# Kernel tuning notes

Measured on AMD Instinct MI355X. Metric: run time of the kernel, lower is better.

The kernel has to match this reference:

```python
import jax, jax.numpy as jnp
import numpy as np

B, T, C = 4, 2048, 1024
H = 16
D = C // H  # head_dim = 64


def setup_inputs() -> dict:
    key = jax.random.key(0)
    k1, k2, k3, k4, k5 = jax.random.split(key, 5)
    s = 0.02
    return {
        "x": jax.random.normal(k1, (B, T, C), dtype=jnp.float32),
        "W_qkv": jax.random.normal(k2, (C, 3 * C), dtype=jnp.float32) * s,
        "b_qkv": jax.random.normal(k3, (3 * C,), dtype=jnp.float32) * s,
        "W_o": jax.random.normal(k4, (C, C), dtype=jnp.float32) * s,
        "b_o": jax.random.normal(k5, (C,), dtype=jnp.float32) * s,
    }


def reference(x, W_qkv, b_qkv, W_o, b_o):
    b, t, c = x.shape
    scaling = D ** (-0.5)
    qkv = x @ W_qkv + b_qkv                      # [B,T,3C]
    q, k, v = jnp.split(qkv, 3, axis=-1)         # each [B,T,C]
    q = q.reshape(b, t, H, D).transpose(0, 2, 1, 3)  # [B,H,T,D]
    k = k.reshape(b, t, H, D).transpose(0, 2, 1, 3)
    v = v.reshape(b, t, H, D).transpose(0, 2, 1, 3)
    scores = jnp.einsum("bhqd,bhkd->bhqk", q, k) * scaling  # [B,H,T,T]
    mask = jnp.tril(jnp.ones((t, t), dtype=bool))            # causal
    scores = jnp.where(mask[None, None, :, :], scores, -jnp.inf)
    probs = jax.nn.softmax(scores, axis=-1)
    out = jnp.einsum("bhqk,bhkd->bhqd", probs, v)            # [B,H,T,D]
    out = out.transpose(0, 2, 1, 3).reshape(b, t, c)         # [B,T,C]
    return out @ W_o + b_o
```

## Files before the change

### kernel.cpp

```cpp
#include <hip/hip_runtime.h>
#include <hip/hip_bf16.h>

typedef unsigned short ushort_t;
typedef __attribute__((ext_vector_type(8))) short short8;
typedef __attribute__((ext_vector_type(4))) float floatx4;

#define B_ 4
#define T_ 2048
#define C_ 1024
#define H_ 16
#define D_ 64
#define BT_ (B_ * T_)
#define N3C (3 * C_)

#define KSC 0.18033688011112042f

__device__ __forceinline__ ushort_t f2bf(float f) {
    unsigned u = __float_as_uint(f);
    u += 0x7FFF + ((u >> 16) & 1);
    return (ushort_t)(u >> 16);
}
__device__ __forceinline__ unsigned pack2bf(float a, float b) {
    __hip_bfloat162 h = __float22bfloat162_rn(make_float2(a, b));
    return *(unsigned*)&h;
}

__device__ __forceinline__ void gload16(const ushort_t* g, ushort_t* l) {
    __builtin_amdgcn_global_load_lds((const __attribute__((address_space(1))) void*)g,
                                     (__attribute__((address_space(3))) void*)l, 16, 0, 0);
}

__global__ void convert_x_k(const float* __restrict__ xin, ushort_t* __restrict__ xb) {
    size_t i = ((size_t)blockIdx.x * 256 + threadIdx.x) * 8;
    const float* xf = xin + i;
    float4 a = *(const float4*)xf;
    float4 b = *(const float4*)(xf + 4);
    short8 o;
    o[0] = (short)f2bf(a.x); o[1] = (short)f2bf(a.y);
    o[2] = (short)f2bf(a.z); o[3] = (short)f2bf(a.w);
    o[4] = (short)f2bf(b.x); o[5] = (short)f2bf(b.y);
    o[6] = (short)f2bf(b.z); o[7] = (short)f2bf(b.w);
    *(short8*)&xb[i] = o;
}

__global__ void transpose_k(const float* __restrict__ in, ushort_t* __restrict__ out,
                            int R, int Nc) {
    __shared__ ushort_t t[32][33];
    int bc = blockIdx.x * 32;
    int br = blockIdx.y * 32;
    int lx = threadIdx.x & 31, ly = threadIdx.x >> 5;
#pragma unroll
    for (int i = 0; i < 4; ++i) {
        int r = ly + i * 8;
        t[r][lx] = f2bf(in[(size_t)(br + r) * Nc + bc + lx]);
    }
    __syncthreads();
#pragma unroll
    for (int i = 0; i < 4; ++i) {
        int r = ly + i * 8;
        out[(size_t)(bc + r) * R + br + lx] = t[lx][r];
    }
}

__global__ void vtrans_k(const ushort_t* __restrict__ in, ushort_t* __restrict__ out) {
    __shared__ ushort_t t[32][33];
    int bh = blockIdx.z;
    const ushort_t* I = in + (size_t)bh * T_ * D_;
    ushort_t* O = out + (size_t)bh * D_ * T_;
    int bt = blockIdx.x * 32, bd = blockIdx.y * 32;
    int lx = threadIdx.x & 31, ly = threadIdx.x >> 5;
#pragma unroll
    for (int i = 0; i < 4; ++i) {
        int r = ly + i * 8;
        t[r][lx] = I[(size_t)(bt + r) * D_ + bd + lx];
    }
    __syncthreads();
#pragma unroll
    for (int i = 0; i < 4; ++i) {
        int r = ly + i * 8;
        O[(size_t)(bd + r) * T_ + bt + lx] = t[lx][r];
    }
}

template <int MODE>
__launch_bounds__(256)
__global__ void gemm_bt(const ushort_t* __restrict__ A, const ushort_t* __restrict__ Bt,
                        const float* __restrict__ bias, float* __restrict__ Cout,
                        ushort_t* __restrict__ Qo, ushort_t* __restrict__ Ko,
                        ushort_t* __restrict__ Vo, int M, int N, int K) {
    __shared__ __align__(16) ushort_t Alds[128 * 32];
    __shared__ __align__(16) ushort_t Blds[128 * 32];
    int tid = threadIdx.x;
    int wave = tid >> 6, lane = tid & 63;
    int bm = blockIdx.x * 128, bn = blockIdx.y * 128;
    int wr = (wave >> 1) * 64, wc = (wave & 1) * 64;
    int lm = lane & 15, lk = (lane >> 4) * 8, lq = lane >> 4;

    floatx4 acc[4][4] = {};

    int srow = tid >> 2;
    int scol = (tid & 3) * 8;
    const ushort_t* Ab = A + (size_t)(bm + srow) * K + scol;
    const ushort_t* Bb = Bt + (size_t)(bn + srow) * K + scol;
    ushort_t* Al0 = &Alds[wave * 512];
    ushort_t* Al1 = &Alds[2048 + wave * 512];
    ushort_t* Bl0 = &Blds[wave * 512];
    ushort_t* Bl1 = &Blds[2048 + wave * 512];
    size_t rowskip = (size_t)64 * K;

    for (int k0 = 0; k0 < K; k0 += 32) {
        __syncthreads();
        gload16(Ab + k0, Al0);
        gload16(Ab + k0 + rowskip, Al1);
        gload16(Bb + k0, Bl0);
        gload16(Bb + k0 + rowskip, Bl1);
        __syncthreads();
        short8 af[4], bf[4];
#pragma unroll
        for (int i = 0; i < 4; ++i)
            af[i] = *(const short8*)&Alds[(wr + i * 16 + lm) * 32 + lk];
#pragma unroll
        for (int i = 0; i < 4; ++i)
            bf[i] = *(const short8*)&Blds[(wc + i * 16 + lm) * 32 + lk];
#pragma unroll
        for (int mi = 0; mi < 4; ++mi)
#pragma unroll
            for (int ni = 0; ni < 4; ++ni)
                acc[mi][ni] = __builtin_amdgcn_mfma_f32_16x16x32_bf16(
                    af[mi], bf[ni], acc[mi][ni], 0, 0, 0);
    }

#pragma unroll
    for (int mi = 0; mi < 4; ++mi) {
#pragma unroll
        for (int ni = 0; ni < 4; ++ni) {
            int col = bn + wc + ni * 16 + lm;
            float bv = bias[col];
#pragma unroll
            for (int r = 0; r < 4; ++r) {
                int row = bm + wr + mi * 16 + lq * 4 + r;
                float v = acc[mi][ni][r] + bv;
                if (MODE == 0) {
                    Cout[(size_t)row * N + col] = v;
                } else {
                    int b = row >> 11, t = row & (T_ - 1);
                    int which = col >> 10, c = col & (C_ - 1);
                    int h = c >> 6, d = c & 63;
                    int bh = b * H_ + h;
                    size_t idx = ((size_t)bh * T_ + t) * D_ + d;
                    if (which == 0)
                        Qo[idx] = f2bf(v * KSC);
                    else if (which == 1)
                        Ko[idx] = f2bf(v);
                    else
                        Vo[idx] = f2bf(v);
                }
            }
        }
    }
}

__launch_bounds__(256)
__global__ void attn_k(const ushort_t* __restrict__ Q, const ushort_t* __restrict__ K,
                       const ushort_t* __restrict__ Vt, ushort_t* __restrict__ O) {
    __shared__ __align__(16) ushort_t Klds[64 * 72];
    __shared__ __align__(16) ushort_t Vlds[64 * 72];
    __shared__ __align__(16) ushort_t Plds[4][16 * 72];

    int tid = threadIdx.x, wave = tid >> 6, lane = tid & 63;
    int id = blockIdx.x;
    int xcd = id & 7, bx = (id >> 3) & 15, grp = id >> 7;
    int bh = xcd + 8 * grp;
    int b = bh >> 4, h = bh & 15;
    int lm = lane & 15, lq = lane >> 4;

    const ushort_t* Qp = Q + (size_t)bh * T_ * D_;
    const ushort_t* Kp = K + (size_t)bh * T_ * D_;
    const ushort_t* Vp = Vt + (size_t)bh * D_ * T_;
    ushort_t* Pw = &Plds[wave][0];
    ushort_t* Ob = O + ((size_t)b * T_) * C_ + h * D_;

    int srow = tid >> 2, scol = (tid & 3) * 16;
    const ushort_t* Kg = Kp + (size_t)srow * D_ + scol;
    const ushort_t* Vg = Vp + (size_t)srow * T_ + scol;
    ushort_t* Kl = &Klds[srow * 72 + scol];
    ushort_t* Vl = &Vlds[srow * 72 + scol];

    int prow = lm * 72 + lq * 4;
    int pread = lm * 72 + lq * 8;

    short8 onesf = {};
    if (lm == 0) {
#pragma unroll
        for (int j = 0; j < 8; ++j) onesf[j] = (short)0x3F80;
    }

#pragma unroll
    for (int pass = 0; pass < 2; ++pass) {
        int band = pass ? (31 - bx) : bx;
        int m0 = band * 64 + wave * 16;

        short8 qf0 = *(const short8*)&Qp[(size_t)(m0 + lm) * D_ + lq * 8];
        short8 qf1 = *(const short8*)&Qp[(size_t)(m0 + lm) * D_ + 32 + lq * 8];

        floatx4 oacc[5] = {};

        int ntw = band + 1;
        short8 kr0 = *(const short8*)Kg;
        short8 kr1 = *(const short8*)(Kg + 8);
        short8 vr0 = *(const short8*)Vg;
        short8 vr1 = *(const short8*)(Vg + 8);

        for (int it = 0; it < ntw; ++it) {
            __syncthreads();
            *(short8*)Kl = kr0;
            *(short8*)(Kl + 8) = kr1;
            *(short8*)Vl = vr0;
            *(short8*)(Vl + 8) = vr1;
            __syncthreads();

            if (it + 1 < ntw) {
                const ushort_t* kn = Kg + (size_t)(it + 1) * 64 * D_;
                const ushort_t* vn = Vg + (it + 1) * 64;
                kr0 = *(const short8*)kn;
                kr1 = *(const short8*)(kn + 8);
                vr0 = *(const short8*)vn;
                vr1 = *(const short8*)(vn + 8);
            }

            short8 kf[4][2], vf[4][2];
#pragma unroll
            for (int nt = 0; nt < 4; ++nt) {
                kf[nt][0] = *(const short8*)&Klds[(nt * 16 + lm) * 72 + lq * 8];
                kf[nt][1] = *(const short8*)&Klds[(nt * 16 + lm) * 72 + 32 + lq * 8];
            }

            floatx4 st[4] = {};
#pragma unroll
            for (int nt = 0; nt < 4; ++nt) {
                st[nt] = __builtin_amdgcn_mfma_f32_16x16x32_bf16(kf[nt][0], qf0, st[nt], 0, 0, 0);
                st[nt] = __builtin_amdgcn_mfma_f32_16x16x32_bf16(kf[nt][1], qf1, st[nt], 0, 0, 0);
            }

#pragma unroll
            for (int dt = 0; dt < 4; ++dt) {
                vf[dt][0] = *(const short8*)&Vlds[(dt * 16 + lm) * 72 + lq * 8];
                vf[dt][1] = *(const short8*)&Vlds[(dt * 16 + lm) * 72 + 32 + lq * 8];
            }

            int kv0 = it * 64;
            if (it == ntw - 1) {
                int mg = m0 + lm;
#pragma unroll
                for (int nt = 0; nt < 4; ++nt)
#pragma unroll
                    for (int r = 0; r < 4; ++r) {
                        int kvg = kv0 + nt * 16 + lq * 4 + r;
                        if (kvg > mg) st[nt][r] = -__builtin_inff();
                    }
            }

#pragma unroll
            for (int nt = 0; nt < 4; ++nt) {
                uint2 pk;
                pk.x = pack2bf(exp2f(st[nt][0]), exp2f(st[nt][1]));
                pk.y = pack2bf(exp2f(st[nt][2]), exp2f(st[nt][3]));
                *(uint2*)&Pw[prow + nt * 16] = pk;
            }

            asm volatile("s_waitcnt lgkmcnt(0)" ::: "memory");

            short8 pb0 = *(const short8*)&Pw[pread];
            short8 pb1 = *(const short8*)&Pw[pread + 32];
#pragma unroll
            for (int dt = 0; dt < 4; ++dt) {
                oacc[dt] = __builtin_amdgcn_mfma_f32_16x16x32_bf16(vf[dt][0], pb0, oacc[dt], 0, 0, 0);
                oacc[dt] = __builtin_amdgcn_mfma_f32_16x16x32_bf16(vf[dt][1], pb1, oacc[dt], 0, 0, 0);
            }
            oacc[4] = __builtin_amdgcn_mfma_f32_16x16x32_bf16(onesf, pb0, oacc[4], 0, 0, 0);
            oacc[4] = __builtin_amdgcn_mfma_f32_16x16x32_bf16(onesf, pb1, oacc[4], 0, 0, 0);
        }

        float li = __shfl(oacc[4][0], lm, 64);
        float inv = 1.0f / li;
        int tg = m0 + lm;
#pragma unroll
        for (int dt = 0; dt < 4; ++dt) {
            uint2 pk;
            pk.x = pack2bf(oacc[dt][0] * inv, oacc[dt][1] * inv);
            pk.y = pack2bf(oacc[dt][2] * inv, oacc[dt][3] * inv);
            *(uint2*)&Ob[(size_t)tg * C_ + dt * 16 + lq * 4] = pk;
        }
    }
}

extern "C" void kernel_launch(void* const* d_in, const int* in_sizes, int n_in,
                              void* d_out, int out_size, void* d_ws, size_t ws_size,
                              hipStream_t stream) {
    const float* x    = (const float*)d_in[0];
    const float* Wqkv = (const float*)d_in[1];
    const float* bqkv = (const float*)d_in[2];
    const float* Wo   = (const float*)d_in[3];
    const float* bo   = (const float*)d_in[4];

    ushort_t* ws = (ushort_t*)d_ws;
    ushort_t* WqkvT = ws;
    ushort_t* WoT   = WqkvT + (size_t)N3C * C_;
    ushort_t* Xb    = WoT + (size_t)C_ * C_;
    ushort_t* Qs    = Xb + (size_t)BT_ * C_;
    ushort_t* Ks    = Qs + (size_t)BT_ * C_;
    ushort_t* Vs    = Ks + (size_t)BT_ * C_;
    ushort_t* Attn  = Vs + (size_t)BT_ * C_;

    convert_x_k<<<BT_ * C_ / (256 * 8), 256, 0, stream>>>(x, Xb);
    transpose_k<<<dim3(N3C / 32, C_ / 32), 256, 0, stream>>>(Wqkv, WqkvT, C_, N3C);
    transpose_k<<<dim3(C_ / 32, C_ / 32), 256, 0, stream>>>(Wo, WoT, C_, C_);
    gemm_bt<1><<<dim3(BT_ / 128, N3C / 128), 256, 0, stream>>>(
        Xb, WqkvT, bqkv, nullptr, Qs, Ks, Attn, BT_, N3C, C_);
    vtrans_k<<<dim3(T_ / 32, D_ / 32, B_ * H_), 256, 0, stream>>>(Attn, Vs);
    attn_k<<<1024, 256, 0, stream>>>(Qs, Ks, Vs, Attn);
    gemm_bt<0><<<dim3(BT_ / 128, C_ / 128), 256, 0, stream>>>(
        Attn, WoT, bo, (float*)d_out, nullptr, nullptr, nullptr, BT_, C_, C_);
}
```

Before: 288.9 us.

## Replace LDS P round-trip with permlane swaps and launch one band per block

The attention kernel now rearranges the bf16 probability tile between MFMA layouts with permlane32/permlane16 swap instructions instead of writing it to shared memory and reading it back. This removes the P LDS buffer and a waitcnt stall. The grid also becomes one causal band per block (2048 blocks), ordered longest band first, instead of pairing short and long bands in one block. This trades the built-in load balance of pairing for more blocks and lower LDS use.

```diff
diff --git a/kernel.cpp b/kernel.cpp
--- a/kernel.cpp
+++ b/kernel.cpp
@@ -4,6 +4,8 @@
 typedef unsigned short ushort_t;
 typedef __attribute__((ext_vector_type(8))) short short8;
 typedef __attribute__((ext_vector_type(4))) float floatx4;
+typedef __attribute__((ext_vector_type(2))) unsigned uint2v;
+typedef __attribute__((ext_vector_type(4))) unsigned uint4v;
 
 #define B_ 4
 #define T_ 2048
@@ -165,19 +167,18 @@
                        const ushort_t* __restrict__ Vt, ushort_t* __restrict__ O) {
     __shared__ __align__(16) ushort_t Klds[64 * 72];
     __shared__ __align__(16) ushort_t Vlds[64 * 72];
-    __shared__ __align__(16) ushort_t Plds[4][16 * 72];
 
     int tid = threadIdx.x, wave = tid >> 6, lane = tid & 63;
     int id = blockIdx.x;
-    int xcd = id & 7, bx = (id >> 3) & 15, grp = id >> 7;
-    int bh = xcd + 8 * grp;
+    int xcd = id & 7, j = id >> 3;
+    int band = 31 - (j & 31);
+    int bh = xcd + 8 * (j >> 5);
     int b = bh >> 4, h = bh & 15;
     int lm = lane & 15, lq = lane >> 4;
 
     const ushort_t* Qp = Q + (size_t)bh * T_ * D_;
     const ushort_t* Kp = K + (size_t)bh * T_ * D_;
     const ushort_t* Vp = Vt + (size_t)bh * D_ * T_;
-    ushort_t* Pw = &Plds[wave][0];
     ushort_t* Ob = O + ((size_t)b * T_) * C_ + h * D_;
 
     int srow = tid >> 2, scol = (tid & 3) * 16;
@@ -186,111 +187,113 @@
     ushort_t* Kl = &Klds[srow * 72 + scol];
     ushort_t* Vl = &Vlds[srow * 72 + scol];
 
-    int prow = lm * 72 + lq * 4;
-    int pread = lm * 72 + lq * 8;
-
     short8 onesf = {};
     if (lm == 0) {
 #pragma unroll
-        for (int j = 0; j < 8; ++j) onesf[j] = (short)0x3F80;
-    }
-
-#pragma unroll
-    for (int pass = 0; pass < 2; ++pass) {
-        int band = pass ? (31 - bx) : bx;
-        int m0 = band * 64 + wave * 16;
-
-        short8 qf0 = *(const short8*)&Qp[(size_t)(m0 + lm) * D_ + lq * 8];
-        short8 qf1 = *(const short8*)&Qp[(size_t)(m0 + lm) * D_ + 32 + lq * 8];
-
-        floatx4 oacc[5] = {};
-
-        int ntw = band + 1;
-        short8 kr0 = *(const short8*)Kg;
-        short8 kr1 = *(const short8*)(Kg + 8);
-        short8 vr0 = *(const short8*)Vg;
-        short8 vr1 = *(const short8*)(Vg + 8);
-
-        for (int it = 0; it < ntw; ++it) {
-            __syncthreads();
-            *(short8*)Kl = kr0;
-            *(short8*)(Kl + 8) = kr1;
-            *(short8*)Vl = vr0;
-            *(short8*)(Vl + 8) = vr1;
-            __syncthreads();
-
-            if (it + 1 < ntw) {
-                const ushort_t* kn = Kg + (size_t)(it + 1) * 64 * D_;
-                const ushort_t* vn = Vg + (it + 1) * 64;
-                kr0 = *(const short8*)kn;
-                kr1 = *(const short8*)(kn + 8);
-                vr0 = *(const short8*)vn;
-                vr1 = *(const short8*)(vn + 8);
-            }
-
-            short8 kf[4][2], vf[4][2];
-#pragma unroll
-            for (int nt = 0; nt < 4; ++nt) {
-                kf[nt][0] = *(const short8*)&Klds[(nt * 16 + lm) * 72 + lq * 8];
-                kf[nt][1] = *(const short8*)&Klds[(nt * 16 + lm) * 72 + 32 + lq * 8];
-            }
-
-            floatx4 st[4] = {};
-#pragma unroll
-            for (int nt = 0; nt < 4; ++nt) {
-                st[nt] = __builtin_amdgcn_mfma_f32_16x16x32_bf16(kf[nt][0], qf0, st[nt], 0, 0, 0);
-                st[nt] = __builtin_amdgcn_mfma_f32_16x16x32_bf16(kf[nt][1], qf1, st[nt], 0, 0, 0);
-            }
-
-#pragma unroll
-            for (int dt = 0; dt < 4; ++dt) {
-                vf[dt][0] = *(const short8*)&Vlds[(dt * 16 + lm) * 72 + lq * 8];
-                vf[dt][1] = *(const short8*)&Vlds[(dt * 16 + lm) * 72 + 32 + lq * 8];
-            }
-
-            int kv0 = it * 64;
-            if (it == ntw - 1) {
-                int mg = m0 + lm;
-#pragma unroll
-                for (int nt = 0; nt < 4; ++nt)
-#pragma unroll
-                    for (int r = 0; r < 4; ++r) {
-                        int kvg = kv0 + nt * 16 + lq * 4 + r;
-                        if (kvg > mg) st[nt][r] = -__builtin_inff();
-                    }
-            }
-
-#pragma unroll
-            for (int nt = 0; nt < 4; ++nt) {
-                uint2 pk;
-                pk.x = pack2bf(exp2f(st[nt][0]), exp2f(st[nt][1]));
-                pk.y = pack2bf(exp2f(st[nt][2]), exp2f(st[nt][3]));
-                *(uint2*)&Pw[prow + nt * 16] = pk;
-            }
-
-            asm volatile("s_waitcnt lgkmcnt(0)" ::: "memory");
-
-            short8 pb0 = *(const short8*)&Pw[pread];
-            short8 pb1 = *(const short8*)&Pw[pread + 32];
-#pragma unroll
-            for (int dt = 0; dt < 4; ++dt) {
-                oacc[dt] = __builtin_amdgcn_mfma_f32_16x16x32_bf16(vf[dt][0], pb0, oacc[dt], 0, 0, 0);
-                oacc[dt] = __builtin_amdgcn_mfma_f32_16x16x32_bf16(vf[dt][1], pb1, oacc[dt], 0, 0, 0);
-            }
-            oacc[4] = __builtin_amdgcn_mfma_f32_16x16x32_bf16(onesf, pb0, oacc[4], 0, 0, 0);
-            oacc[4] = __builtin_amdgcn_mfma_f32_16x16x32_bf16(onesf, pb1, oacc[4], 0, 0, 0);
-        }
-
-        float li = __shfl(oacc[4][0], lm, 64);
-        float inv = 1.0f / li;
-        int tg = m0 + lm;
+        for (int jj = 0; jj < 8; ++jj) onesf[jj] = (short)0x3F80;
+    }
+
+    int m0 = band * 64 + wave * 16;
+
+    short8 qf0 = *(const short8*)&Qp[(size_t)(m0 + lm) * D_ + lq * 8];
+    short8 qf1 = *(const short8*)&Qp[(size_t)(m0 + lm) * D_ + 32 + lq * 8];
+
+    floatx4 oacc[5] = {};
+
+    int ntw = band + 1;
+    short8 kr0 = *(const short8*)Kg;
+    short8 kr1 = *(const short8*)(Kg + 8);
+    short8 vr0 = *(const short8*)Vg;
+    short8 vr1 = *(const short8*)(Vg + 8);
+
+    for (int it = 0; it < ntw; ++it) {
+        __syncthreads();
+        *(short8*)Kl = kr0;
+        *(short8*)(Kl + 8) = kr1;
+        *(short8*)Vl = vr0;
+        *(short8*)(Vl + 8) = vr1;
+        __syncthreads();
+
+        if (it + 1 < ntw) {
+            const ushort_t* kn = Kg + (size_t)(it + 1) * 64 * D_;
+            const ushort_t* vn = Vg + (it + 1) * 64;
+            kr0 = *(const short8*)kn;
+            kr1 = *(const short8*)(kn + 8);
+            vr0 = *(const short8*)vn;
+            vr1 = *(const short8*)(vn + 8);
+        }
+
+        short8 kf[4][2], vf[4][2];
+#pragma unroll
+        for (int nt = 0; nt < 4; ++nt) {
+            kf[nt][0] = *(const short8*)&Klds[(nt * 16 + lm) * 72 + lq * 8];
+            kf[nt][1] = *(const short8*)&Klds[(nt * 16 + lm) * 72 + 32 + lq * 8];
+        }
+
+        floatx4 st[4] = {};
+#pragma unroll
+        for (int nt = 0; nt < 4; ++nt) {
+            st[nt] = __builtin_amdgcn_mfma_f32_16x16x32_bf16(kf[nt][0], qf0, st[nt], 0, 0, 0);
+            st[nt] = __builtin_amdgcn_mfma_f32_16x16x32_bf16(kf[nt][1], qf1, st[nt], 0, 0, 0);
+        }
+
 #pragma unroll
         for (int dt = 0; dt < 4; ++dt) {
-            uint2 pk;
-            pk.x = pack2bf(oacc[dt][0] * inv, oacc[dt][1] * inv);
-            pk.y = pack2bf(oacc[dt][2] * inv, oacc[dt][3] * inv);
-            *(uint2*)&Ob[(size_t)tg * C_ + dt * 16 + lq * 4] = pk;
-        }
+            vf[dt][0] = *(const short8*)&Vlds[(dt * 16 + lm) * 72 + lq * 8];
+            vf[dt][1] = *(const short8*)&Vlds[(dt * 16 + lm) * 72 + 32 + lq * 8];
+        }
+
+        int kv0 = it * 64;
+        if (it == ntw - 1) {
+            int mg = m0 + lm;
+#pragma unroll
+            for (int nt = 0; nt < 4; ++nt)
+#pragma unroll
+                for (int r = 0; r < 4; ++r) {
+                    int kvg = kv0 + nt * 16 + lq * 4 + r;
+                    if (kvg > mg) st[nt][r] = -__builtin_inff();
+                }
+        }
+
+        unsigned e0 = pack2bf(exp2f(st[0][0]), exp2f(st[0][1]));
+        unsigned e1 = pack2bf(exp2f(st[0][2]), exp2f(st[0][3]));
+        unsigned e2 = pack2bf(exp2f(st[1][0]), exp2f(st[1][1]));
+        unsigned e3 = pack2bf(exp2f(st[1][2]), exp2f(st[1][3]));
+        unsigned e4 = pack2bf(exp2f(st[2][0]), exp2f(st[2][1]));
+        unsigned e5 = pack2bf(exp2f(st[2][2]), exp2f(st[2][3]));
+        unsigned e6 = pack2bf(exp2f(st[3][0]), exp2f(st[3][1]));
+        unsigned e7 = pack2bf(exp2f(st[3][2]), exp2f(st[3][3]));
+
+        uint2v ra = __builtin_amdgcn_permlane32_swap(e0, e2, false, false);
+        uint2v wa = __builtin_amdgcn_permlane16_swap(ra[0], ra[1], false, false);
+        uint2v rb = __builtin_amdgcn_permlane32_swap(e1, e3, false, false);
+        uint2v wb = __builtin_amdgcn_permlane16_swap(rb[0], rb[1], false, false);
+        uint2v rc = __builtin_amdgcn_permlane32_swap(e4, e6, false, false);
+        uint2v wc = __builtin_amdgcn_permlane16_swap(rc[0], rc[1], false, false);
+        uint2v rd = __builtin_amdgcn_permlane32_swap(e5, e7, false, false);
+        uint2v wd = __builtin_amdgcn_permlane16_swap(rd[0], rd[1], false, false);
+
+        short8 pb0 = __builtin_bit_cast(short8, (uint4v){wa[0], wb[0], wa[1], wb[1]});
+        short8 pb1 = __builtin_bit_cast(short8, (uint4v){wc[0], wd[0], wc[1], wd[1]});
+
+#pragma unroll
+        for (int dt = 0; dt < 4; ++dt) {
+            oacc[dt] = __builtin_amdgcn_mfma_f32_16x16x32_bf16(vf[dt][0], pb0, oacc[dt], 0, 0, 0);
+            oacc[dt] = __builtin_amdgcn_mfma_f32_16x16x32_bf16(vf[dt][1], pb1, oacc[dt], 0, 0, 0);
+        }
+        oacc[4] = __builtin_amdgcn_mfma_f32_16x16x32_bf16(onesf, pb0, oacc[4], 0, 0, 0);
+        oacc[4] = __builtin_amdgcn_mfma_f32_16x16x32_bf16(onesf, pb1, oacc[4], 0, 0, 0);
+    }
+
+    float li = __shfl(oacc[4][0], lm, 64);
+    float inv = 1.0f / li;
+    int tg = m0 + lm;
+#pragma unroll
+    for (int dt = 0; dt < 4; ++dt) {
+        uint2 pk;
+        pk.x = pack2bf(oacc[dt][0] * inv, oacc[dt][1] * inv);
+        pk.y = pack2bf(oacc[dt][2] * inv, oacc[dt][3] * inv);
+        *(uint2*)&Ob[(size_t)tg * C_ + dt * 16 + lq * 4] = pk;
     }
 }
 
@@ -318,7 +321,7 @@
     gemm_bt<1><<<dim3(BT_ / 128, N3C / 128), 256, 0, stream>>>(
         Xb, WqkvT, bqkv, nullptr, Qs, Ks, Attn, BT_, N3C, C_);
     vtrans_k<<<dim3(T_ / 32, D_ / 32, B_ * H_), 256, 0, stream>>>(Attn, Vs);
-    attn_k<<<1024, 256, 0, stream>>>(Qs, Ks, Vs, Attn);
+    attn_k<<<2048, 256, 0, stream>>>(Qs, Ks, Vs, Attn);
     gemm_bt<0><<<dim3(BT_ / 128, C_ / 128), 256, 0, stream>>>(
         Attn, WoT, bo, (float*)d_out, nullptr, nullptr, nullptr, BT_, C_, C_);
 }
```

New measurement: 290.4 us. No clear change (+0.5%).
